# Performance work log

Hardware: AMD Instinct MI355X
Metric: run time of the kernel (lower is better)

The kernel has to match this reference:

```python
import jax, jax.numpy as jnp
import numpy as np

B, C, H, W = 4, 64, 128, 128
NUM_HEAD = 1
SCALE = (C // NUM_HEAD) ** (-0.5)


def setup_inputs():
    key = jax.random.key(0)
    ks = jax.random.split(key, 32)
    def nrm(k, shape, s=0.05):
        return jax.random.normal(k, shape, jnp.float32) * s
    inp = {"x": jax.random.normal(ks[0], (B, C, H, W), jnp.float32)}
    i = 1
    for wn, bn in [("Wq", "bq"), ("Wk", "bk"), ("Wv", "bv"), ("Wl", "bl"), ("Wo", "bo"), ("Wp", "bp")]:
        inp[wn] = nrm(ks[i], (C, C)); i += 1
        inp[bn] = nrm(ks[i], (C,)); i += 1
    inp["sch_dw"] = nrm(ks[i], (C, 1, 5, 1)); i += 1
    inp["sch_dwb"] = nrm(ks[i], (C,)); i += 1
    inp["sch_pw"] = nrm(ks[i], (C, C, 1, 1)); i += 1
    inp["sch_pwb"] = nrm(ks[i], (C,)); i += 1
    inp["scv_dw"] = nrm(ks[i], (C, 1, 1, 5)); i += 1
    inp["scv_dwb"] = nrm(ks[i], (C,)); i += 1
    inp["scv_pw"] = nrm(ks[i], (C, C, 1, 1)); i += 1
    inp["scv_pwb"] = nrm(ks[i], (C,)); i += 1
    inp["convh_w"] = nrm(ks[i], (C, C, 1, 1)); i += 1
    inp["convh_b"] = nrm(ks[i], (C,)); i += 1
    inp["dsc_dw"] = nrm(ks[i], (C, 1, 3, 3)); i += 1
    inp["dsc_dwb"] = nrm(ks[i], (C,)); i += 1
    inp["dsc_pw"] = nrm(ks[i], (C, C, 1, 1)); i += 1
    inp["dsc_pwb"] = nrm(ks[i], (C,)); i += 1
    inp["ln_g"] = jnp.ones((C,), jnp.float32)
    inp["ln_b"] = jnp.zeros((C,), jnp.float32)
    return inp


def _linear(x, w, b):  # x [B,N,C], w [C,C] (torch Linear convention: y = x @ w.T + b)
    return x @ w.T + b


def _dwconv(x, w, b, pad):  # depthwise: x [B,C,H,W], w [C,1,kh,kw]
    y = jax.lax.conv_general_dilated(x, w, (1, 1), [(pad[0], pad[0]), (pad[1], pad[1])],
                                     dimension_numbers=("NCHW", "OIHW", "NCHW"),
                                     feature_group_count=x.shape[1])
    return y + b[None, :, None, None]


def _pwconv(x, w, b):  # 1x1 conv: w [Co,Ci,1,1]
    return jnp.einsum("bchw,oc->bohw", x, w[:, :, 0, 0]) + b[None, :, None, None]


def _attn(q, k, v):  # [B,N,C] each; dense NxN softmax attention
    a = jax.nn.softmax(jnp.einsum("bnc,bmc->bnm", q, k) * SCALE, axis=-1)
    return jnp.einsum("bnm,bmc->bnc", a, v)


def _up2_bilinear(x):  # bilinear, scale 2, align_corners=True
    Bb, Cc, Hh, Ww = x.shape
    def coords(n):
        s = jnp.linspace(0.0, n - 1.0, 2 * n)
        i0 = jnp.floor(s).astype(jnp.int32)
        i1 = jnp.minimum(i0 + 1, n - 1)
        return i0, i1, (s - i0).astype(x.dtype)
    y0, y1, wy = coords(Hh)
    x0, x1, wx = coords(Ww)
    r = x[:, :, y0, :] * (1.0 - wy)[None, None, :, None] + x[:, :, y1, :] * wy[None, None, :, None]
    return r[:, :, :, x0] * (1.0 - wx) + r[:, :, :, x1] * wx


def _forward(x, Wq, bq, Wk, bk, Wv, bv, Wl, bl, Wo, bo, Wp, bp,
             sch_dw, sch_dwb, sch_pw, sch_pwb, scv_dw, scv_dwb, scv_pw, scv_pwb,
             convh_w, convh_b, dsc_dw, dsc_dwb, dsc_pw, dsc_pwb, ln_g, ln_b):
    Bb, Cc, Hh, Ww = x.shape
    # AvgPool2d(2,2)
    xp = x.reshape(Bb, Cc, Hh // 2, 2, Ww // 2, 2).mean((3, 5))
    Hp, Wp_ = Hh // 2, Ww // 2
    N = Hp * Wp_
    # forward_lpg: GAP-gated self-attention producing low-freq prompt
    gap = xp.mean((2, 3), keepdims=True)
    xg = (gap * xp).reshape(Bb, Cc, N).transpose(0, 2, 1)  # [B,N,C]
    q = _linear(xg, Wq, bq); k = _linear(xg, Wk, bk); v = _linear(xg, Wv, bv)
    prompt_l = _linear(_attn(q, k, v), Wl, bl).transpose(0, 2, 1).reshape(Bb, Cc, Hp, Wp_)
    # forward_hpg: separable strip-conv branches -> high-freq prompt
    x_h = _pwconv(jax.nn.gelu(_dwconv(xp, sch_dw, sch_dwb, (2, 0)), approximate=False), sch_pw, sch_pwb)
    x_v = _pwconv(jax.nn.gelu(_dwconv(xp, scv_dw, scv_dwb, (0, 2)), approximate=False), scv_pw, scv_pwb)
    prompt_h = _pwconv(x_h + x_v, convh_w, convh_b)
    # forward_pgc: cross-attention Q=high, K=low, V=linear(x)
    x_V = _linear(xp.reshape(Bb, Cc, N).transpose(0, 2, 1), Wo, bo)
    x_K = prompt_l.reshape(Bb, Cc, N).transpose(0, 2, 1)
    x_Q = prompt_h.reshape(Bb, Cc, N).transpose(0, 2, 1)
    prompt = _attn(x_Q, x_K, x_V)
    prompt = _linear(prompt, Wp, bp) + x_V
    # LayerNorm over channel dim
    mu = prompt.mean(-1, keepdims=True)
    var = jnp.mean((prompt - mu) ** 2, axis=-1, keepdims=True)
    p_norm = (prompt - mu) / jnp.sqrt(var + 1e-5) * ln_g + ln_b
    p_norm = p_norm.transpose(0, 2, 1).reshape(Bb, Cc, Hp, Wp_)
    # dsc: depthwise 3x3 -> GELU -> 1x1, residual
    out = _pwconv(jax.nn.gelu(_dwconv(p_norm, dsc_dw, dsc_dwb, (1, 1)), approximate=False), dsc_pw, dsc_pwb) + p_norm
    return _up2_bilinear(out)


def reference(x, Wq, bq, Wk, bk, Wv, bv, Wl, bl, Wo, bo, Wp, bp,
              sch_dw, sch_dwb, sch_pw, sch_pwb, scv_dw, scv_dwb, scv_pw, scv_pwb,
              convh_w, convh_b, dsc_dw, dsc_dwb, dsc_pw, dsc_pwb, ln_g, ln_b):
    return _forward(x, Wq, bq, Wk, bk, Wv, bv, Wl, bl, Wo, bo, Wp, bp,
                    sch_dw, sch_dwb, sch_pw, sch_pwb, scv_dw, scv_dwb, scv_pw, scv_pwb,
                    convh_w, convh_b, dsc_dw, dsc_dwb, dsc_pw, dsc_pwb, ln_g, ln_b)
```

## Files before the change

### kernel.cpp

```cpp
#include <hip/hip_runtime.h>
#include <math.h>

#define Bn 4
#define Cn 64
#define Np 4096
#define NSPLIT 4
#define SCALE2 0.18033688011112042f

typedef unsigned short ushort_t;
typedef __attribute__((ext_vector_type(4))) float f32x4;
typedef __attribute__((ext_vector_type(8))) short bf16x8;
typedef __attribute__((ext_vector_type(4))) short bf16x4;

__device__ __forceinline__ float gelu_exact(float x) {
    return 0.5f * x * (1.0f + erff(x * 0.70710678118654752440f));
}
__device__ __forceinline__ ushort_t f2bf(float f) {
    unsigned int u = __float_as_uint(f);
    u += 0x7fffu + ((u >> 16) & 1u);
    return (ushort_t)(u >> 16);
}
__device__ __forceinline__ ushort_t f2bf_tr(float f) {
    return (ushort_t)(__float_as_uint(f) >> 16);
}
__device__ __forceinline__ float bf2f(ushort_t h) {
    return __uint_as_float(((unsigned int)h) << 16);
}
__device__ __forceinline__ void gload_lds16(const ushort_t* g, ushort_t* l) {
    __builtin_amdgcn_global_load_lds(
        (const __attribute__((address_space(1))) void*)g,
        (__attribute__((address_space(3))) void*)l, 16, 0, 0);
}
__device__ __forceinline__ bf16x8 cvt8(const float v[8]) {
    bf16x8 r;
    #pragma unroll
    for (int j = 0; j < 8; ++j) r[j] = (short)f2bf(v[j]);
    return r;
}
__device__ __forceinline__ void gemm16(const bf16x8 af[2], const float* __restrict__ W,
                                       int l16, int quad, f32x4* acc) {
    #pragma unroll
    for (int cb = 0; cb < 4; ++cb) {
        #pragma unroll
        for (int ks = 0; ks < 2; ++ks) {
            const float* p = W + (cb * 16 + l16) * 64 + ks * 32 + quad * 8;
            float v[8];
            #pragma unroll
            for (int j = 0; j < 8; ++j) v[j] = p[j];
            acc[cb] = __builtin_amdgcn_mfma_f32_16x16x32_bf16(af[ks], cvt8(v), acc[cb], 0, 0, 0);
        }
    }
}
__device__ __forceinline__ void gemm16T(const bf16x8 af[2], const float* __restrict__ W,
                                        int l16, int quad, f32x4* acc) {
    #pragma unroll
    for (int cb = 0; cb < 4; ++cb) {
        #pragma unroll
        for (int ks = 0; ks < 2; ++ks) {
            const float* p = W + (cb * 16 + l16) * 64 + ks * 32 + quad * 8;
            float v[8];
            #pragma unroll
            for (int j = 0; j < 8; ++j) v[j] = p[j];
            acc[cb] = __builtin_amdgcn_mfma_f32_16x16x32_bf16(cvt8(v), af[ks], acc[cb], 0, 0, 0);
        }
    }
}
__device__ __forceinline__ void aload(const float* xs, int row, int quad, bf16x8 af[2]) {
    #pragma unroll
    for (int ks = 0; ks < 2; ++ks) {
        float v[8];
        #pragma unroll
        for (int j = 0; j < 8; ++j) v[j] = xs[(ks * 32 + quad * 8 + j) * 65 + row];
        af[ks] = cvt8(v);
    }
}
__device__ __forceinline__ void stage_bchw(const float* __restrict__ X, int b, int n0, int t,
                                           float* xs) {
    #pragma unroll
    for (int u = 0; u < 16; ++u) {
        int idx = t + u * 256;
        int c = idx >> 6, nl = idx & 63;
        xs[c * 65 + nl] = X[((size_t)(b * Cn + c)) * Np + n0 + nl];
    }
}
__device__ __forceinline__ void stage_comb(const ushort_t* __restrict__ OpB, const float* linv,
                                           int b, int n0, int t, float* xs) {
    const size_t SS = (size_t)Bn * Np * Cn;
    #pragma unroll
    for (int u = 0; u < 16; ++u) {
        int idx = t + u * 256;
        int nl = idx >> 6, c = idx & 63;
        size_t gi = ((size_t)(b * Np + n0 + nl)) * Cn + c;
        float s = bf2f(OpB[gi]) + bf2f(OpB[SS + gi]) +
                  bf2f(OpB[2 * SS + gi]) + bf2f(OpB[3 * SS + gi]);
        xs[c * 65 + nl] = s * linv[nl];
    }
}
__device__ __forceinline__ void store_bnc_T(ushort_t* __restrict__ Y, int b, int n, int quad,
                                            const f32x4* acc, const float* __restrict__ bias,
                                            float mult) {
    #pragma unroll
    for (int cb = 0; cb < 4; ++cb) {
        int o0 = cb * 16 + quad * 4;
        ushort4 pk;
        pk.x = f2bf((acc[cb][0] + bias[o0 + 0]) * mult);
        pk.y = f2bf((acc[cb][1] + bias[o0 + 1]) * mult);
        pk.z = f2bf((acc[cb][2] + bias[o0 + 2]) * mult);
        pk.w = f2bf((acc[cb][3] + bias[o0 + 3]) * mult);
        *(ushort4*)(Y + ((size_t)(b * Np + n)) * Cn + o0) = pk;
    }
}
__device__ __forceinline__ void store_bchw_bf16(ushort_t* __restrict__ Y, int b, int nb, int l16,
                                                const f32x4* acc, const float* __restrict__ bias) {
    #pragma unroll
    for (int cb = 0; cb < 4; ++cb) {
        int col = cb * 16 + l16;
        float bb = bias[col];
        ushort4 pk;
        pk.x = f2bf(acc[cb][0] + bb); pk.y = f2bf(acc[cb][1] + bb);
        pk.z = f2bf(acc[cb][2] + bb); pk.w = f2bf(acc[cb][3] + bb);
        *(ushort4*)(Y + ((size_t)(b * Cn + col)) * Np + nb) = pk;
    }
}

__global__ void avgpool_kernel(const float* __restrict__ x, float* __restrict__ xp,
                               float* __restrict__ gap4k,
                               const float* __restrict__ convh_w, const float* __restrict__ convh_b,
                               const float* __restrict__ sch_pw, const float* __restrict__ sch_pwb,
                               const float* __restrict__ scv_pw, const float* __restrict__ scv_pwb,
                               float* __restrict__ Wc1, float* __restrict__ Wc2,
                               float* __restrict__ bcv) {
    if (blockIdx.x < 4096) {
        int idx = blockIdx.x * 256 + threadIdx.x;
        int j  = idx & 63;
        int i  = (idx >> 6) & 63;
        int bc = idx >> 12;
        const float* p = x + ((size_t)bc * 128 + 2 * i) * 128 + 2 * j;
        float v = 0.25f * (p[0] + p[1] + p[128] + p[129]);
        xp[idx] = v;
        float s = v;
        #pragma unroll
        for (int off = 1; off < 64; off <<= 1) s += __shfl_xor(s, off, 64);
        __shared__ float sm[4];
        if ((threadIdx.x & 63) == 0) sm[threadIdx.x >> 6] = s;
        __syncthreads();
        if (threadIdx.x == 0) gap4k[blockIdx.x] = sm[0] + sm[1] + sm[2] + sm[3];
    } else {
        int g = (blockIdx.x - 4096) * 256 + threadIdx.x;
        int sel = g >> 12, idx = g & 4095;
        int o = idx >> 6, c = idx & 63;
        const float* pw = sel ? scv_pw : sch_pw;
        float acc = 0.f;
        #pragma unroll 8
        for (int m = 0; m < 64; ++m) acc += convh_w[o * 64 + m] * pw[m * 64 + c];
        (sel ? Wc2 : Wc1)[idx] = acc * SCALE2;
        if (g < 64) {
            float ab = convh_b[g];
            for (int m = 0; m < 64; ++m) ab += convh_w[g * 64 + m] * (sch_pwb[m] + scv_pwb[m]);
            bcv[g] = ab * SCALE2;
        }
    }
}

__global__ __launch_bounds__(256) void qkv_dw_kernel(
    const float* __restrict__ xp, const float* __restrict__ gap4k,
    const float* __restrict__ Wq, const float* __restrict__ bq,
    const float* __restrict__ Wk, const float* __restrict__ bk,
    const float* __restrict__ Wv, const float* __restrict__ bv,
    const float* __restrict__ Wo, const float* __restrict__ bo,
    ushort_t* __restrict__ qb, ushort_t* __restrict__ kb, ushort_t* __restrict__ vb,
    float* __restrict__ xV, ushort_t* __restrict__ xVtb,
    const float* __restrict__ wv5, const float* __restrict__ bv5,
    const float* __restrict__ wh5, const float* __restrict__ bh5,
    ushort_t* __restrict__ gh, ushort_t* __restrict__ gv) {
    int b = blockIdx.y, t = threadIdx.x;
    if (blockIdx.x >= 64) {
        int part = blockIdx.x - 64;
        int e = part * 1024 + t * 4;
        size_t base = (size_t)b * (Cn * Np) + e;
        int c = e >> 12, i = (e >> 6) & 63, j = e & 63;
        const float* p = xp + ((size_t)(b * Cn + c)) * Np;
        float accV[4], accH[4];
        #pragma unroll
        for (int k = 0; k < 4; ++k) { accV[k] = bv5[c]; accH[k] = bh5[c]; }
        #pragma unroll
        for (int d = 0; d < 5; ++d) {
            int ii = i + d - 2;
            if (ii >= 0 && ii < 64) {
                #pragma unroll
                for (int k = 0; k < 4; ++k) accV[k] += wv5[c * 5 + d] * p[ii * 64 + j + k];
            }
        }
        #pragma unroll
        for (int k = 0; k < 4; ++k) {
            #pragma unroll
            for (int d = 0; d < 5; ++d) {
                int jj = j + k + d - 2;
                if (jj >= 0 && jj < 64) accH[k] += wh5[c * 5 + d] * p[i * 64 + jj];
            }
        }
        ushort4 ph, pv_;
        ph.x = f2bf(gelu_exact(accV[0])); ph.y = f2bf(gelu_exact(accV[1]));
        ph.z = f2bf(gelu_exact(accV[2])); ph.w = f2bf(gelu_exact(accV[3]));
        pv_.x = f2bf(gelu_exact(accH[0])); pv_.y = f2bf(gelu_exact(accH[1]));
        pv_.z = f2bf(gelu_exact(accH[2])); pv_.w = f2bf(gelu_exact(accH[3]));
        *(ushort4*)(gh + base) = ph;
        *(ushort4*)(gv + base) = pv_;
        return;
    }
    __shared__ float xs[64 * 65];
    __shared__ float gl[64];
    int n0 = blockIdx.x * 64;
    int wv_ = t >> 6, lane = t & 63, l16 = lane & 15, quad = lane >> 4;
    stage_bchw(xp, b, n0, t, xs);
    if (t < 64) {
        float s = 0.f;
        #pragma unroll
        for (int u = 0; u < 16; ++u) s += gap4k[(b * 64 + t) * 16 + u];
        gl[t] = s * (1.f / 4096.f);
    }
    __syncthreads();
    int row = wv_ * 16 + l16;
    int n   = n0 + wv_ * 16 + l16;
    int nb  = n0 + wv_ * 16 + quad * 4;
    bf16x8 ar[2], ag[2];
    #pragma unroll
    for (int ks = 0; ks < 2; ++ks) {
        float vr[8], vg[8];
        #pragma unroll
        for (int j = 0; j < 8; ++j) {
            int k = ks * 32 + quad * 8 + j;
            float xv = xs[k * 65 + row];
            vr[j] = xv; vg[j] = xv * gl[k];
        }
        ar[ks] = cvt8(vr); ag[ks] = cvt8(vg);
    }
    f32x4 acc[4];
    #pragma unroll
    for (int cb = 0; cb < 4; ++cb) acc[cb] = (f32x4){0.f, 0.f, 0.f, 0.f};
    gemm16T(ag, Wq, l16, quad, acc);
    store_bnc_T(qb, b, n, quad, acc, bq, SCALE2);
    #pragma unroll
    for (int cb = 0; cb < 4; ++cb) acc[cb] = (f32x4){0.f, 0.f, 0.f, 0.f};
    gemm16T(ag, Wk, l16, quad, acc);
    store_bnc_T(kb, b, n, quad, acc, bk, 1.f);
    #pragma unroll
    for (int cb = 0; cb < 4; ++cb) acc[cb] = (f32x4){0.f, 0.f, 0.f, 0.f};
    gemm16(ag, Wv, l16, quad, acc);
    store_bchw_bf16(vb, b, nb, l16, acc, bv);
    #pragma unroll
    for (int cb = 0; cb < 4; ++cb) acc[cb] = (f32x4){0.f, 0.f, 0.f, 0.f};
    gemm16(ar, Wo, l16, quad, acc);
    #pragma unroll
    for (int cb = 0; cb < 4; ++cb) {
        int col = cb * 16 + l16;
        float bb = bo[col];
        ushort4 pk;
        float y0 = acc[cb][0] + bb, y1 = acc[cb][1] + bb, y2 = acc[cb][2] + bb, y3 = acc[cb][3] + bb;
        xV[((size_t)(b * Np + nb + 0)) * Cn + col] = y0;
        xV[((size_t)(b * Np + nb + 1)) * Cn + col] = y1;
        xV[((size_t)(b * Np + nb + 2)) * Cn + col] = y2;
        xV[((size_t)(b * Np + nb + 3)) * Cn + col] = y3;
        pk.x = f2bf(y0); pk.y = f2bf(y1); pk.z = f2bf(y2); pk.w = f2bf(y3);
        *(ushort4*)(xVtb + ((size_t)(b * Cn + col)) * Np + nb) = pk;
    }
}

__device__ __forceinline__ void attn_body(
    int xblk, int b, const ushort_t* __restrict__ Qb, const ushort_t* __restrict__ Kb,
    const ushort_t* __restrict__ Vtb, ushort_t* __restrict__ OpB, float* __restrict__ Lpart,
    ushort_t* smem) {
    ushort_t* kt0 = smem;
    ushort_t* vt0 = smem + 8192;
    int split = xblk >> 6;
    int qt    = xblk & 63;
    int n0    = qt * 64;
    int t     = threadIdx.x;
    int wave  = t >> 6, lane = t & 63;
    int l16   = lane & 15, quad = lane >> 4;

    const ushort_t* qp = Qb + ((size_t)(b * Np) + n0 + wave * 16 + l16) * Cn + quad * 8;
    bf16x8 aq0 = *(const bf16x8*)(qp);
    bf16x8 aq1 = *(const bf16x8*)(qp + 32);

    f32x4 oa[4];
    float psum = 0.f;
    #pragma unroll
    for (int db = 0; db < 4; ++db) oa[db] = (f32x4){0.f, 0.f, 0.f, 0.f};

    int lrow = lane >> 3;
    int kvbase = split * (Np / NSPLIT);
    const ushort_t* Kg = Qb == nullptr ? nullptr : Kb + ((size_t)b * Np) * Cn;
    const ushort_t* Vg = Vtb + ((size_t)b * Cn) * Np;

    auto stage = [&](int buf, int k0) {
        int wh = wave & 1;
        if (wave < 2) {
            ushort_t* dst = kt0 + buf * 4096 + wh * 2048;
            #pragma unroll
            for (int u = 0; u < 4; ++u) {
                int r = wh * 32 + u * 8 + lrow;
                int jsw = ((lane & 7) ^ lrow ^ (wh * 4 + u)) & 7;
                gload_lds16(Kg + ((size_t)(k0 + r)) * Cn + jsw * 8, dst + u * 512);
            }
        } else {
            ushort_t* dst = vt0 + buf * 4096 + wh * 2048;
            #pragma unroll
            for (int u = 0; u < 4; ++u) {
                int d = wh * 32 + u * 8 + lrow;
                int jsw = ((lane & 7) ^ lrow ^ (wh * 4 + u)) & 7;
                gload_lds16(Vg + (size_t)d * Np + k0 + jsw * 8, dst + u * 512);
            }
        }
    };
    const int NT = (Np / NSPLIT) / 64;
    stage(0, kvbase);
    __syncthreads();

    for (int m = 0; m < NT; ++m) {
        int cur = m & 1;
        if (m + 1 < NT) stage(1 - cur, kvbase + (m + 1) * 64);
        const ushort_t* ktc = kt0 + cur * 4096;
        const ushort_t* vtc = vt0 + cur * 4096;

        f32x4 sa[4];
        #pragma unroll
        for (int cb = 0; cb < 4; ++cb) sa[cb] = (f32x4){0.f, 0.f, 0.f, 0.f};
        #pragma unroll
        for (int cb = 0; cb < 4; ++cb) {
            int key = ((l16 & 7) ^ (cb * 2 + (l16 >> 3))) & 7;
            const ushort_t* krow = ktc + (cb * 16 + l16) * 64;
            bf16x8 bk0 = *(const bf16x8*)(krow + ((quad    ) ^ key) * 8);
            bf16x8 bk1 = *(const bf16x8*)(krow + ((quad + 4) ^ key) * 8);
            sa[cb] = __builtin_amdgcn_mfma_f32_16x16x32_bf16(bk0, aq0, sa[cb], 0, 0, 0);
            sa[cb] = __builtin_amdgcn_mfma_f32_16x16x32_bf16(bk1, aq1, sa[cb], 0, 0, 0);
        }
        bf16x4 pb[4];
        #pragma unroll
        for (int cb = 0; cb < 4; ++cb) {
            float p0 = exp2f(sa[cb][0]), p1 = exp2f(sa[cb][1]);
            float p2 = exp2f(sa[cb][2]), p3 = exp2f(sa[cb][3]);
            psum += (p0 + p1) + (p2 + p3);
            bf16x4 pk;
            pk[0] = (short)f2bf_tr(p0); pk[1] = (short)f2bf_tr(p1);
            pk[2] = (short)f2bf_tr(p2); pk[3] = (short)f2bf_tr(p3);
            pb[cb] = pk;
        }
        #pragma unroll
        for (int kc = 0; kc < 4; ++kc) {
            #pragma unroll
            for (int db = 0; db < 4; ++db) {
                int d = db * 16 + l16;
                int key = ((l16 & 7) ^ (db * 2 + (l16 >> 3))) & 7;
                int phys = (kc * 2 + (quad >> 1)) ^ key;
                const ushort_t* va = vtc + d * 64 + phys * 8 + (quad & 1) * 4;
                bf16x4 av = *(const bf16x4*)va;
                oa[db] = __builtin_amdgcn_mfma_f32_16x16x16bf16_1k(av, pb[kc], oa[db], 0, 0, 0);
            }
        }
        __syncthreads();
    }
    psum += __shfl_xor(psum, 16, 64);
    psum += __shfl_xor(psum, 32, 64);
    size_t obase = ((size_t)(split * Bn + b)) * Np;
    int n = n0 + wave * 16 + l16;
    if (quad == 0) Lpart[obase + n] = psum;
    #pragma unroll
    for (int db = 0; db < 4; ++db) {
        ushort4 pk;
        pk.x = f2bf(oa[db][0]); pk.y = f2bf(oa[db][1]);
        pk.z = f2bf(oa[db][2]); pk.w = f2bf(oa[db][3]);
        *(ushort4*)(OpB + (obase + n) * Cn + db * 16 + quad * 4) = pk;
    }
}

__device__ __forceinline__ void hpg_body(
    int tile, int b, const ushort_t* __restrict__ gh, const ushort_t* __restrict__ gv,
    const float* __restrict__ Wc1, const float* __restrict__ Wc2, const float* __restrict__ bcv,
    ushort_t* __restrict__ xQb, ushort_t* smem) {
    ushort_t* xs1 = smem;
    ushort_t* xs2 = smem + 4608;
    int n0 = tile * 64, t = threadIdx.x;
    int wv_ = t >> 6, lane = t & 63, l16 = lane & 15, quad = lane >> 4;
    #pragma unroll
    for (int u = 0; u < 4; ++u) {
        int lin = u * 256 + t;
        int c = lin >> 4, nl4 = (lin & 15) * 4;
        size_t gi = ((size_t)(b * Cn + c)) * Np + n0 + nl4;
        ushort4 g1 = *(const ushort4*)(gh + gi);
        ushort4 g2 = *(const ushort4*)(gv + gi);
        xs1[(nl4 + 0) * 72 + c] = g1.x; xs1[(nl4 + 1) * 72 + c] = g1.y;
        xs1[(nl4 + 2) * 72 + c] = g1.z; xs1[(nl4 + 3) * 72 + c] = g1.w;
        xs2[(nl4 + 0) * 72 + c] = g2.x; xs2[(nl4 + 1) * 72 + c] = g2.y;
        xs2[(nl4 + 2) * 72 + c] = g2.z; xs2[(nl4 + 3) * 72 + c] = g2.w;
    }
    __syncthreads();
    int row = wv_ * 16 + l16;
    bf16x8 a1[2], a2[2];
    #pragma unroll
    for (int ks = 0; ks < 2; ++ks) {
        a1[ks] = *(const bf16x8*)(xs1 + row * 72 + ks * 32 + quad * 8);
        a2[ks] = *(const bf16x8*)(xs2 + row * 72 + ks * 32 + quad * 8);
    }
    f32x4 acc[4];
    #pragma unroll
    for (int cb = 0; cb < 4; ++cb) acc[cb] = (f32x4){0.f, 0.f, 0.f, 0.f};
    gemm16T(a1, Wc1, l16, quad, acc);
    gemm16T(a2, Wc2, l16, quad, acc);
    store_bnc_T(xQb, b, n0 + wv_ * 16 + l16, quad, acc, bcv, 1.f);
}

__global__ __launch_bounds__(256) void attn_hpg_kernel(
    const ushort_t* __restrict__ Qb, const ushort_t* __restrict__ Kb,
    const ushort_t* __restrict__ Vtb, ushort_t* __restrict__ OpB, float* __restrict__ Lpart,
    const ushort_t* __restrict__ gh, const ushort_t* __restrict__ gv,
    const float* __restrict__ Wc1, const float* __restrict__ Wc2,
    const float* __restrict__ bcv, ushort_t* __restrict__ xQb) {
    __shared__ ushort_t smem[16384];
    int b = blockIdx.y;
    if (blockIdx.x < 256)
        attn_body(blockIdx.x, b, Qb, Kb, Vtb, OpB, Lpart, smem);
    else
        hpg_body(blockIdx.x - 256, b, gh, gv, Wc1, Wc2, bcv, xQb, smem);
}

__global__ __launch_bounds__(256) void wl_mfma(
    const ushort_t* __restrict__ OpB, const float* __restrict__ Lp,
    const float* __restrict__ Wl, const float* __restrict__ bl, ushort_t* __restrict__ xKb) {
    __shared__ float xs[64 * 65];
    __shared__ float linv[64];
    int b = blockIdx.y, n0 = blockIdx.x * 64, t = threadIdx.x;
    int wv_ = t >> 6, lane = t & 63, l16 = lane & 15, quad = lane >> 4;
    if (t < 64) {
        size_t li = (size_t)b * Np + n0 + t;
        const size_t LS = (size_t)Bn * Np;
        linv[t] = 1.f / (Lp[li] + Lp[LS + li] + Lp[2 * LS + li] + Lp[3 * LS + li]);
    }
    __syncthreads();
    stage_comb(OpB, linv, b, n0, t, xs);
    __syncthreads();
    bf16x8 af[2];
    aload(xs, wv_ * 16 + l16, quad, af);
    f32x4 acc[4];
    #pragma unroll
    for (int cb = 0; cb < 4; ++cb) acc[cb] = (f32x4){0.f, 0.f, 0.f, 0.f};
    gemm16T(af, Wl, l16, quad, acc);
    store_bnc_T(xKb, b, n0 + wv_ * 16 + l16, quad, acc, bl, 1.f);
}

__global__ __launch_bounds__(256) void linln_mfma(
    const ushort_t* __restrict__ OpB, const float* __restrict__ Lp,
    const float* __restrict__ Wp, const float* __restrict__ bp,
    const float* __restrict__ xV, const float* __restrict__ g, const float* __restrict__ beta,
    float* __restrict__ out) {
    __shared__ float xs[64 * 65];
    __shared__ float linv[64];
    int b = blockIdx.y, n0 = blockIdx.x * 64, t = threadIdx.x;
    int wv_ = t >> 6, lane = t & 63, l16 = lane & 15, quad = lane >> 4;
    if (t < 64) {
        size_t li = (size_t)b * Np + n0 + t;
        const size_t LS = (size_t)Bn * Np;
        linv[t] = 1.f / (Lp[li] + Lp[LS + li] + Lp[2 * LS + li] + Lp[3 * LS + li]);
    }
    __syncthreads();
    stage_comb(OpB, linv, b, n0, t, xs);
    __syncthreads();
    bf16x8 af[2];
    aload(xs, wv_ * 16 + l16, quad, af);
    f32x4 acc[4];
    #pragma unroll
    for (int cb = 0; cb < 4; ++cb) acc[cb] = (f32x4){0.f, 0.f, 0.f, 0.f};
    gemm16(af, Wp, l16, quad, acc);
    int nb = n0 + wv_ * 16 + quad * 4;
    float vals[4][4], gc[4], bec[4];
    #pragma unroll
    for (int cb = 0; cb < 4; ++cb) {
        int col = cb * 16 + l16;
        float bb = bp[col];
        gc[cb] = g[col]; bec[cb] = beta[col];
        #pragma unroll
        for (int r = 0; r < 4; ++r)
            vals[cb][r] = acc[cb][r] + bb + xV[((size_t)(b * Np + nb + r)) * Cn + col];
    }
    f32x4 yn[4];
    #pragma unroll
    for (int r = 0; r < 4; ++r) {
        float s = 0.f, s2 = 0.f;
        #pragma unroll
        for (int cb = 0; cb < 4; ++cb) { s += vals[cb][r]; s2 += vals[cb][r] * vals[cb][r]; }
        #pragma unroll
        for (int off = 1; off < 16; off <<= 1) {
            s  += __shfl_xor(s, off, 64);
            s2 += __shfl_xor(s2, off, 64);
        }
        float mu  = s * (1.f / 64.f);
        float var = s2 * (1.f / 64.f) - mu * mu;
        float ivs = rsqrtf(var + 1e-5f);
        #pragma unroll
        for (int cb = 0; cb < 4; ++cb)
            yn[cb][r] = (vals[cb][r] - mu) * ivs * gc[cb] + bec[cb];
    }
    #pragma unroll
    for (int cb = 0; cb < 4; ++cb)
        *(f32x4*)(out + ((size_t)(b * Cn + cb * 16 + l16)) * Np + nb) = yn[cb];
}

__global__ void dw3x3_gelu_kernel(const float* __restrict__ xin, const float* __restrict__ w,
                                  const float* __restrict__ bias, float* __restrict__ out) {
    int idx = blockIdx.x * 256 + threadIdx.x;
    int j = idx & 63, i = (idx >> 6) & 63, bc = idx >> 12, c = bc & 63;
    const float* p = xin + (size_t)bc * Np;
    float acc = bias[c];
    #pragma unroll
    for (int dy = 0; dy < 3; ++dy) {
        int ii = i + dy - 1;
        if (ii < 0 || ii >= 64) continue;
        #pragma unroll
        for (int dx = 0; dx < 3; ++dx) {
            int jj = j + dx - 1;
            if (jj < 0 || jj >= 64) continue;
            acc += w[c * 9 + dy * 3 + dx] * p[ii * 64 + jj];
        }
    }
    out[idx] = gelu_exact(acc);
}

__global__ __launch_bounds__(256) void dsc_mfma(
    const float* __restrict__ X, const float* __restrict__ W, const float* __restrict__ bias,
    const float* __restrict__ res, float* __restrict__ out) {
    __shared__ float xs[64 * 65];
    int b = blockIdx.y, n0 = blockIdx.x * 64, t = threadIdx.x;
    int wv_ = t >> 6, lane = t & 63, l16 = lane & 15, quad = lane >> 4;
    stage_bchw(X, b, n0, t, xs);
    __syncthreads();
    bf16x8 af[2];
    aload(xs, wv_ * 16 + l16, quad, af);
    f32x4 acc[4];
    #pragma unroll
    for (int cb = 0; cb < 4; ++cb) acc[cb] = (f32x4){0.f, 0.f, 0.f, 0.f};
    gemm16(af, W, l16, quad, acc);
    int nb = n0 + wv_ * 16 + quad * 4;
    #pragma unroll
    for (int cb = 0; cb < 4; ++cb) {
        int col = cb * 16 + l16;
        float bb = bias[col];
        size_t oi = ((size_t)(b * Cn + col)) * Np + nb;
        f32x4 rv = *(const f32x4*)(res + oi);
        f32x4 v4;
        #pragma unroll
        for (int r = 0; r < 4; ++r) v4[r] = acc[cb][r] + bb + rv[r];
        *(f32x4*)(out + oi) = v4;
    }
}

__global__ void upsample_kernel(const float* __restrict__ in, float* __restrict__ out) {
    int idx = blockIdx.x * 256 + threadIdx.x;
    int x  = idx & 127;
    int y  = (idx >> 7) & 127;
    int bc = idx >> 14;
    float sy = y * (63.f / 127.f);
    float sx = x * (63.f / 127.f);
    int y0 = (int)sy, x0 = (int)sx;
    float fy = sy - y0, fx = sx - x0;
    int y1 = min(y0 + 1, 63), x1 = min(x0 + 1, 63);
    const float* p = in + (size_t)bc * Np;
    float v00 = p[y0 * 64 + x0], v01 = p[y0 * 64 + x1];
    float v10 = p[y1 * 64 + x0], v11 = p[y1 * 64 + x1];
    out[idx] = (v00 * (1.f - fx) + v01 * fx) * (1.f - fy) +
               (v10 * (1.f - fx) + v11 * fx) * fy;
}

extern "C" void kernel_launch(void* const* d_in, const int* in_sizes, int n_in,
                              void* d_out, int out_size, void* d_ws, size_t ws_size,
                              hipStream_t stream) {
    const float* x       = (const float*)d_in[0];
    const float* Wq      = (const float*)d_in[1];
    const float* bq      = (const float*)d_in[2];
    const float* Wk      = (const float*)d_in[3];
    const float* bk      = (const float*)d_in[4];
    const float* Wv      = (const float*)d_in[5];
    const float* bv      = (const float*)d_in[6];
    const float* Wl      = (const float*)d_in[7];
    const float* bl      = (const float*)d_in[8];
    const float* Wo      = (const float*)d_in[9];
    const float* bo      = (const float*)d_in[10];
    const float* Wp      = (const float*)d_in[11];
    const float* bp      = (const float*)d_in[12];
    const float* sch_dw  = (const float*)d_in[13];
    const float* sch_dwb = (const float*)d_in[14];
    const float* sch_pw  = (const float*)d_in[15];
    const float* sch_pwb = (const float*)d_in[16];
    const float* scv_dw  = (const float*)d_in[17];
    const float* scv_dwb = (const float*)d_in[18];
    const float* scv_pw  = (const float*)d_in[19];
    const float* scv_pwb = (const float*)d_in[20];
    const float* convh_w = (const float*)d_in[21];
    const float* convh_b = (const float*)d_in[22];
    const float* dsc_dw  = (const float*)d_in[23];
    const float* dsc_dwb = (const float*)d_in[24];
    const float* dsc_pw  = (const float*)d_in[25];
    const float* dsc_pwb = (const float*)d_in[26];
    const float* ln_g    = (const float*)d_in[27];
    const float* ln_b    = (const float*)d_in[28];

    float* ws = (float*)d_ws;
    const size_t SZ = (size_t)Bn * Np * Cn;
    float* xp   = ws;
    float* xV   = ws + SZ;
    ushort_t* ghb = (ushort_t*)(ws + 2 * SZ);
    ushort_t* gh  = ghb;
    ushort_t* gv  = ghb + SZ;
    float* f2   = ws + 2 * SZ;
    ushort_t* bws  = (ushort_t*)(ws + 3 * SZ);
    ushort_t* qb   = bws;
    ushort_t* kb_  = bws + SZ;
    ushort_t* vb   = bws + 2 * SZ;
    ushort_t* xKb  = bws + 3 * SZ;
    ushort_t* xVtb = bws + 4 * SZ;
    ushort_t* xQb  = bws + 5 * SZ;
    ushort_t* OpB  = (ushort_t*)(ws + 6 * SZ);
    float* gap4k  = ws + 8 * SZ;
    float* Lpart  = gap4k + 4096;
    float* Wc1  = Lpart + (size_t)NSPLIT * Bn * Np;
    float* Wc2  = Wc1 + 4096;
    float* bcv  = Wc2 + 4096;

    dim3 g64(64, Bn);

    avgpool_kernel<<<4096 + 32, 256, 0, stream>>>(x, xp, gap4k,
                                                  convh_w, convh_b, sch_pw, sch_pwb,
                                                  scv_pw, scv_pwb, Wc1, Wc2, bcv);
    qkv_dw_kernel<<<dim3(64 + 256, Bn), 256, 0, stream>>>(
        xp, gap4k, Wq, bq, Wk, bk, Wv, bv, Wo, bo,
        qb, kb_, vb, xV, xVtb, sch_dw, sch_dwb, scv_dw, scv_dwb, gh, gv);
    attn_hpg_kernel<<<dim3(256 + 64, Bn), 256, 0, stream>>>(
        qb, kb_, vb, OpB, Lpart, gh, gv, Wc1, Wc2, bcv, xQb);
    wl_mfma<<<g64, 256, 0, stream>>>(OpB, Lpart, Wl, bl, xKb);
    attn_hpg_kernel<<<dim3(256, Bn), 256, 0, stream>>>(
        xQb, xKb, xVtb, OpB, Lpart, gh, gv, Wc1, Wc2, bcv, xQb);
    linln_mfma<<<g64, 256, 0, stream>>>(OpB, Lpart, Wp, bp, xV, ln_g, ln_b, xp);
    dw3x3_gelu_kernel<<<4096, 256, 0, stream>>>(xp, dsc_dw, dsc_dwb, xV);
    dsc_mfma<<<g64, 256, 0, stream>>>(xV, dsc_pw, dsc_pwb, xp, f2);
    upsample_kernel<<<16384, 256, 0, stream>>>(f2, (float*)d_out);
}
```

Measured before the change: 243.9 us.

## Process two query tiles per attention block, fuse dwconv+pwconv, vectorize upsample

Each attention block now handles 128 queries in two groups, so every staged K/V tile is reused twice and the grid is halved, with a launch bound of two blocks per CU. The separate depthwise 3x3 GELU kernel is fused into the 1x1 conv kernel by staging a three-row halo in shared memory, which removes an intermediate global round trip. The upsample kernel writes four outputs per thread with a vector store. The cost is higher register pressure in attention, fewer attention blocks to fill the GPU, and a large shared-memory footprint in the fused conv kernel.

Measured after the change: 260.2 us. +6.7%, slower.

```diff
diff --git a/kernel.cpp b/kernel.cpp
--- a/kernel.cpp
+++ b/kernel.cpp
@@ -272,25 +272,31 @@
     ushort_t* smem) {
     ushort_t* kt0 = smem;
     ushort_t* vt0 = smem + 8192;
-    int split = xblk >> 6;
-    int qt    = xblk & 63;
-    int n0    = qt * 64;
+    int split = xblk >> 5;
+    int qt    = xblk & 31;
+    int n0    = qt * 128;
     int t     = threadIdx.x;
     int wave  = t >> 6, lane = t & 63;
     int l16   = lane & 15, quad = lane >> 4;
 
-    const ushort_t* qp = Qb + ((size_t)(b * Np) + n0 + wave * 16 + l16) * Cn + quad * 8;
-    bf16x8 aq0 = *(const bf16x8*)(qp);
-    bf16x8 aq1 = *(const bf16x8*)(qp + 32);
-
-    f32x4 oa[4];
-    float psum = 0.f;
-    #pragma unroll
-    for (int db = 0; db < 4; ++db) oa[db] = (f32x4){0.f, 0.f, 0.f, 0.f};
+    bf16x8 aq[2][2];
+    #pragma unroll
+    for (int qg = 0; qg < 2; ++qg) {
+        const ushort_t* qp = Qb + ((size_t)(b * Np) + n0 + qg * 64 + wave * 16 + l16) * Cn + quad * 8;
+        aq[qg][0] = *(const bf16x8*)(qp);
+        aq[qg][1] = *(const bf16x8*)(qp + 32);
+    }
+
+    f32x4 oa[2][4];
+    float psum[2] = {0.f, 0.f};
+    #pragma unroll
+    for (int qg = 0; qg < 2; ++qg)
+        #pragma unroll
+        for (int db = 0; db < 4; ++db) oa[qg][db] = (f32x4){0.f, 0.f, 0.f, 0.f};
 
     int lrow = lane >> 3;
     int kvbase = split * (Np / NSPLIT);
-    const ushort_t* Kg = Qb == nullptr ? nullptr : Kb + ((size_t)b * Np) * Cn;
+    const ushort_t* Kg = Kb + ((size_t)b * Np) * Cn;
     const ushort_t* Vg = Vtb + ((size_t)b * Cn) * Np;
 
     auto stage = [&](int buf, int k0) {
@@ -323,28 +329,36 @@
         const ushort_t* ktc = kt0 + cur * 4096;
         const ushort_t* vtc = vt0 + cur * 4096;
 
-        f32x4 sa[4];
-        #pragma unroll
-        for (int cb = 0; cb < 4; ++cb) sa[cb] = (f32x4){0.f, 0.f, 0.f, 0.f};
+        f32x4 sa[2][4];
+        #pragma unroll
+        for (int qg = 0; qg < 2; ++qg)
+            #pragma unroll
+            for (int cb = 0; cb < 4; ++cb) sa[qg][cb] = (f32x4){0.f, 0.f, 0.f, 0.f};
         #pragma unroll
         for (int cb = 0; cb < 4; ++cb) {
             int key = ((l16 & 7) ^ (cb * 2 + (l16 >> 3))) & 7;
             const ushort_t* krow = ktc + (cb * 16 + l16) * 64;
             bf16x8 bk0 = *(const bf16x8*)(krow + ((quad    ) ^ key) * 8);
             bf16x8 bk1 = *(const bf16x8*)(krow + ((quad + 4) ^ key) * 8);
-            sa[cb] = __builtin_amdgcn_mfma_f32_16x16x32_bf16(bk0, aq0, sa[cb], 0, 0, 0);
-            sa[cb] = __builtin_amdgcn_mfma_f32_16x16x32_bf16(bk1, aq1, sa[cb], 0, 0, 0);
-        }
-        bf16x4 pb[4];
-        #pragma unroll
-        for (int cb = 0; cb < 4; ++cb) {
-            float p0 = exp2f(sa[cb][0]), p1 = exp2f(sa[cb][1]);
-            float p2 = exp2f(sa[cb][2]), p3 = exp2f(sa[cb][3]);
-            psum += (p0 + p1) + (p2 + p3);
-            bf16x4 pk;
-            pk[0] = (short)f2bf_tr(p0); pk[1] = (short)f2bf_tr(p1);
-            pk[2] = (short)f2bf_tr(p2); pk[3] = (short)f2bf_tr(p3);
-            pb[cb] = pk;
+            #pragma unroll
+            for (int qg = 0; qg < 2; ++qg) {
+                sa[qg][cb] = __builtin_amdgcn_mfma_f32_16x16x32_bf16(bk0, aq[qg][0], sa[qg][cb], 0, 0, 0);
+                sa[qg][cb] = __builtin_amdgcn_mfma_f32_16x16x32_bf16(bk1, aq[qg][1], sa[qg][cb], 0, 0, 0);
+            }
+        }
+        bf16x4 pb[2][4];
+        #pragma unroll
+        for (int qg = 0; qg < 2; ++qg) {
+            #pragma unroll
+            for (int cb = 0; cb < 4; ++cb) {
+                float p0 = exp2f(sa[qg][cb][0]), p1 = exp2f(sa[qg][cb][1]);
+                float p2 = exp2f(sa[qg][cb][2]), p3 = exp2f(sa[qg][cb][3]);
+                psum[qg] += (p0 + p1) + (p2 + p3);
+                bf16x4 pk;
+                pk[0] = (short)f2bf_tr(p0); pk[1] = (short)f2bf_tr(p1);
+                pk[2] = (short)f2bf_tr(p2); pk[3] = (short)f2bf_tr(p3);
+                pb[qg][cb] = pk;
+            }
         }
         #pragma unroll
         for (int kc = 0; kc < 4; ++kc) {
@@ -355,22 +369,27 @@
                 int phys = (kc * 2 + (quad >> 1)) ^ key;
                 const ushort_t* va = vtc + d * 64 + phys * 8 + (quad & 1) * 4;
                 bf16x4 av = *(const bf16x4*)va;
-                oa[db] = __builtin_amdgcn_mfma_f32_16x16x16bf16_1k(av, pb[kc], oa[db], 0, 0, 0);
+                oa[0][db] = __builtin_amdgcn_mfma_f32_16x16x16bf16_1k(av, pb[0][kc], oa[0][db], 0, 0, 0);
+                oa[1][db] = __builtin_amdgcn_mfma_f32_16x16x16bf16_1k(av, pb[1][kc], oa[1][db], 0, 0, 0);
             }
         }
         __syncthreads();
     }
-    psum += __shfl_xor(psum, 16, 64);
-    psum += __shfl_xor(psum, 32, 64);
     size_t obase = ((size_t)(split * Bn + b)) * Np;
-    int n = n0 + wave * 16 + l16;
-    if (quad == 0) Lpart[obase + n] = psum;
-    #pragma unroll
-    for (int db = 0; db < 4; ++db) {
-        ushort4 pk;
-        pk.x = f2bf(oa[db][0]); pk.y = f2bf(oa[db][1]);
-        pk.z = f2bf(oa[db][2]); pk.w = f2bf(oa[db][3]);
-        *(ushort4*)(OpB + (obase + n) * Cn + db * 16 + quad * 4) = pk;
+    #pragma unroll
+    for (int qg = 0; qg < 2; ++qg) {
+        float s = psum[qg];
+        s += __shfl_xor(s, 16, 64);
+        s += __shfl_xor(s, 32, 64);
+        int n = n0 + qg * 64 + wave * 16 + l16;
+        if (quad == 0) Lpart[obase + n] = s;
+        #pragma unroll
+        for (int db = 0; db < 4; ++db) {
+            ushort4 pk;
+            pk.x = f2bf(oa[qg][db][0]); pk.y = f2bf(oa[qg][db][1]);
+            pk.z = f2bf(oa[qg][db][2]); pk.w = f2bf(oa[qg][db][3]);
+            *(ushort4*)(OpB + (obase + n) * Cn + db * 16 + quad * 4) = pk;
+        }
     }
 }
 
@@ -410,7 +429,7 @@
     store_bnc_T(xQb, b, n0 + wv_ * 16 + l16, quad, acc, bcv, 1.f);
 }
 
-__global__ __launch_bounds__(256) void attn_hpg_kernel(
+__global__ __launch_bounds__(256, 2) void attn_hpg_kernel(
     const ushort_t* __restrict__ Qb, const ushort_t* __restrict__ Kb,
     const ushort_t* __restrict__ Vtb, ushort_t* __restrict__ OpB, float* __restrict__ Lpart,
     const ushort_t* __restrict__ gh, const ushort_t* __restrict__ gv,
@@ -418,10 +437,10 @@
     const float* __restrict__ bcv, ushort_t* __restrict__ xQb) {
     __shared__ ushort_t smem[16384];
     int b = blockIdx.y;
-    if (blockIdx.x < 256)
+    if (blockIdx.x < 128)
         attn_body(blockIdx.x, b, Qb, Kb, Vtb, OpB, Lpart, smem);
     else
-        hpg_body(blockIdx.x - 256, b, gh, gv, Wc1, Wc2, bcv, xQb, smem);
+        hpg_body(blockIdx.x - 128, b, gh, gv, Wc1, Wc2, bcv, xQb, smem);
 }
 
 __global__ __launch_bounds__(256) void wl_mfma(
@@ -505,33 +524,39 @@
         *(f32x4*)(out + ((size_t)(b * Cn + cb * 16 + l16)) * Np + nb) = yn[cb];
 }
 
-__global__ void dw3x3_gelu_kernel(const float* __restrict__ xin, const float* __restrict__ w,
-                                  const float* __restrict__ bias, float* __restrict__ out) {
-    int idx = blockIdx.x * 256 + threadIdx.x;
-    int j = idx & 63, i = (idx >> 6) & 63, bc = idx >> 12, c = bc & 63;
-    const float* p = xin + (size_t)bc * Np;
-    float acc = bias[c];
-    #pragma unroll
-    for (int dy = 0; dy < 3; ++dy) {
-        int ii = i + dy - 1;
-        if (ii < 0 || ii >= 64) continue;
-        #pragma unroll
-        for (int dx = 0; dx < 3; ++dx) {
-            int jj = j + dx - 1;
-            if (jj < 0 || jj >= 64) continue;
-            acc += w[c * 9 + dy * 3 + dx] * p[ii * 64 + jj];
-        }
-    }
-    out[idx] = gelu_exact(acc);
-}
-
-__global__ __launch_bounds__(256) void dsc_mfma(
-    const float* __restrict__ X, const float* __restrict__ W, const float* __restrict__ bias,
-    const float* __restrict__ res, float* __restrict__ out) {
+__global__ __launch_bounds__(256) void dsc_fused(
+    const float* __restrict__ pn, const float* __restrict__ dw, const float* __restrict__ dwb,
+    const float* __restrict__ W, const float* __restrict__ bias, float* __restrict__ out) {
+    __shared__ float halo[3 * 4096];
     __shared__ float xs[64 * 65];
-    int b = blockIdx.y, n0 = blockIdx.x * 64, t = threadIdx.x;
+    int b = blockIdx.y, i = blockIdx.x, n0 = i * 64, t = threadIdx.x;
     int wv_ = t >> 6, lane = t & 63, l16 = lane & 15, quad = lane >> 4;
-    stage_bchw(X, b, n0, t, xs);
+    #pragma unroll
+    for (int u = 0; u < 48; ++u) {
+        int lin = t + u * 256;
+        int r = lin >> 12, rest = lin & 4095;
+        int c = rest >> 6, j = rest & 63;
+        int ri = i - 1 + r;
+        halo[lin] = (ri >= 0 && ri < 64)
+            ? pn[((size_t)(b * Cn + c)) * Np + ri * 64 + j] : 0.f;
+    }
+    __syncthreads();
+    #pragma unroll
+    for (int u = 0; u < 16; ++u) {
+        int idx = t + u * 256;
+        int c = idx >> 6, j = idx & 63;
+        const float* hc = halo + c * 64;
+        float acc = dwb[c];
+        #pragma unroll
+        for (int dy = 0; dy < 3; ++dy) {
+            #pragma unroll
+            for (int dx = 0; dx < 3; ++dx) {
+                int jj = j + dx - 1;
+                if (jj >= 0 && jj < 64) acc += dw[c * 9 + dy * 3 + dx] * hc[dy * 4096 + jj];
+            }
+        }
+        xs[c * 65 + j] = gelu_exact(acc);
+    }
     __syncthreads();
     bf16x8 af[2];
     aload(xs, wv_ * 16 + l16, quad, af);
@@ -545,7 +570,7 @@
         int col = cb * 16 + l16;
         float bb = bias[col];
         size_t oi = ((size_t)(b * Cn + col)) * Np + nb;
-        f32x4 rv = *(const f32x4*)(res + oi);
+        f32x4 rv = *(const f32x4*)(pn + oi);
         f32x4 v4;
         #pragma unroll
         for (int r = 0; r < 4; ++r) v4[r] = acc[cb][r] + bb + rv[r];
@@ -555,19 +580,28 @@
 
 __global__ void upsample_kernel(const float* __restrict__ in, float* __restrict__ out) {
     int idx = blockIdx.x * 256 + threadIdx.x;
-    int x  = idx & 127;
-    int y  = (idx >> 7) & 127;
-    int bc = idx >> 14;
+    int x4 = (idx & 31) * 4;
+    int y  = (idx >> 5) & 127;
+    int bc = idx >> 12;
     float sy = y * (63.f / 127.f);
-    float sx = x * (63.f / 127.f);
-    int y0 = (int)sy, x0 = (int)sx;
-    float fy = sy - y0, fx = sx - x0;
-    int y1 = min(y0 + 1, 63), x1 = min(x0 + 1, 63);
-    const float* p = in + (size_t)bc * Np;
-    float v00 = p[y0 * 64 + x0], v01 = p[y0 * 64 + x1];
-    float v10 = p[y1 * 64 + x0], v11 = p[y1 * 64 + x1];
-    out[idx] = (v00 * (1.f - fx) + v01 * fx) * (1.f - fy) +
-               (v10 * (1.f - fx) + v11 * fx) * fy;
+    int y0 = (int)sy;
+    float fy = sy - y0;
+    int y1 = min(y0 + 1, 63);
+    const float* p0 = in + (size_t)bc * Np + y0 * 64;
+    const float* p1 = in + (size_t)bc * Np + y1 * 64;
+    f32x4 o;
+    #pragma unroll
+    for (int k = 0; k < 4; ++k) {
+        int x = x4 + k;
+        float sx = x * (63.f / 127.f);
+        int x0 = (int)sx;
+        float fx = sx - x0;
+        int x1 = min(x0 + 1, 63);
+        float r0 = p0[x0] * (1.f - fx) + p0[x1] * fx;
+        float r1 = p1[x0] * (1.f - fx) + p1[x1] * fx;
+        o[k] = r0 * (1.f - fy) + r1 * fy;
+    }
+    *(f32x4*)(out + ((size_t)bc << 14) + y * 128 + x4) = o;
 }
 
 extern "C" void kernel_launch(void* const* d_in, const int* in_sizes, int n_in,
@@ -633,13 +667,12 @@
     qkv_dw_kernel<<<dim3(64 + 256, Bn), 256, 0, stream>>>(
         xp, gap4k, Wq, bq, Wk, bk, Wv, bv, Wo, bo,
         qb, kb_, vb, xV, xVtb, sch_dw, sch_dwb, scv_dw, scv_dwb, gh, gv);
-    attn_hpg_kernel<<<dim3(256 + 64, Bn), 256, 0, stream>>>(
+    attn_hpg_kernel<<<dim3(128 + 64, Bn), 256, 0, stream>>>(
         qb, kb_, vb, OpB, Lpart, gh, gv, Wc1, Wc2, bcv, xQb);
     wl_mfma<<<g64, 256, 0, stream>>>(OpB, Lpart, Wl, bl, xKb);
-    attn_hpg_kernel<<<dim3(256, Bn), 256, 0, stream>>>(
+    attn_hpg_kernel<<<dim3(128, Bn), 256, 0, stream>>>(
         xQb, xKb, xVtb, OpB, Lpart, gh, gv, Wc1, Wc2, bcv, xQb);
     linln_mfma<<<g64, 256, 0, stream>>>(OpB, Lpart, Wp, bp, xV, ln_g, ln_b, xp);
-    dw3x3_gelu_kernel<<<4096, 256, 0, stream>>>(xp, dsc_dw, dsc_dwb, xV);
-    dsc_mfma<<<g64, 256, 0, stream>>>(xV, dsc_pw, dsc_pwb, xp, f2);
-    upsample_kernel<<<16384, 256, 0, stream>>>(f2, (float*)d_out);
-}
+    dsc_fused<<<g64, 256, 0, stream>>>(xp, dsc_dw, dsc_dwb, dsc_pw, dsc_pwb, f2);
+    upsample_kernel<<<4096, 256, 0, stream>>>(f2, (float*)d_out);
+}
```
